# Kernel tuning notes

Measured on AMD Instinct MI355X. Metric: run time of the kernel, lower is better.

Reference implementation:

```python
import jax, jax.numpy as jnp
import numpy as np

B, S, DIM = 2, 512, 4096
SMAX = 4096
HQ, HKV, HD = 32, 8, 128
REP = HQ // HKV
THETA = 1e6
NEG = -1e9  # stands in for -inf in the causal mask (safe under softmax/vjp)


def setup_inputs() -> dict:
    key = jax.random.key(0)
    ks = jax.random.split(key, 8)
    x = jax.random.normal(ks[0], (B, S, DIM), jnp.float32)
    # RoPE tables (complex freqs_cis represented as cos/sin), rope_theta=1e6
    inv = 1.0 / (THETA ** (np.arange(0, HD, 2, dtype=np.float64) / HD))
    ang = np.arange(SMAX, dtype=np.float64)[:, None] * inv[None, :]
    freqs_cos = jnp.asarray(np.cos(ang), jnp.float32)  # [SMAX, HD//2]
    freqs_sin = jnp.asarray(np.sin(ang), jnp.float32)
    cache = jax.random.normal(ks[1], (2, 1, B, SMAX, HKV, HD), jnp.float32) * 0.02
    i = np.arange(SMAX)
    mask = jnp.asarray(np.where(i[None, :] <= i[:, None], 0.0, NEG), jnp.float32)
    storage_idx = jnp.arange(S, dtype=jnp.int32)
    sc = 0.02
    wq = jax.random.normal(ks[2], (HQ * HD, DIM), jnp.float32) * sc
    wk = jax.random.normal(ks[3], (HKV * HD, DIM), jnp.float32) * sc
    wv = jax.random.normal(ks[4], (HKV * HD, DIM), jnp.float32) * sc
    wo = jax.random.normal(ks[5], (DIM, HQ * HD), jnp.float32) * sc
    return {"x": x, "freqs_cos": freqs_cos, "freqs_sin": freqs_sin, "cache": cache,
            "mask": mask, "storage_idx": storage_idx, "wq": wq, "wk": wk, "wv": wv, "wo": wo}


def _rope(t, c, s):
    # t: [B,S,H,HD]; consecutive pairs (2i, 2i+1) form complex numbers
    tr = t.reshape(*t.shape[:-1], -1, 2)
    a, b = tr[..., 0], tr[..., 1]
    o0 = a * c - b * s
    o1 = a * s + b * c
    return jnp.stack([o0, o1], axis=-1).reshape(t.shape)


def reference(x, freqs_cos, freqs_sin, cache, mask, storage_idx, wq, wk, wv, wo):
    bsz, seqlen, _ = x.shape
    hd = cache.shape[-1]
    hkv = cache.shape[-2]
    hq = wq.shape[0] // hd
    rep = hq // hkv
    xq = (x @ wq.T).reshape(bsz, seqlen, hq, hd)
    xk = (x @ wk.T).reshape(bsz, seqlen, hkv, hd)
    xv = (x @ wv.T).reshape(bsz, seqlen, hkv, hd)
    c = freqs_cos[storage_idx][None, :, None, :]  # [1,S,1,HD//2]
    s = freqs_sin[storage_idx][None, :, None, :]
    xq = _rope(xq, c, s)
    xk = _rope(xk, c, s)
    # rotating-cache write (index_copy along seq dim of cache[0/1, li])
    k_cache = cache[0, 0].at[:, storage_idx].set(xk)  # [B,SMAX,HKV,HD]
    v_cache = cache[1, 0].at[:, storage_idx].set(xv)
    keys = jnp.repeat(k_cache, rep, axis=2)    # GQA expand -> [B,SMAX,HQ,HD]
    values = jnp.repeat(v_cache, rep, axis=2)
    # NOTE: faithful to source: scores = QK^T / (head_dim ** -0.5)
    scores = jnp.einsum('bqhd,bkhd->bhqk', xq, keys) / (hd ** -0.5)
    scores = scores + mask[storage_idx][None, None, :, :]
    probs = jax.nn.softmax(scores.astype(jnp.float32), axis=-1).astype(xq.dtype)
    out = jnp.einsum('bhqk,bkhd->bqhd', probs, values).reshape(bsz, seqlen, hq * hd)
    return out @ wo.T
```

## Files before the change

kernel.cpp:

```cpp
#include <hip/hip_runtime.h>

#define Bn   2
#define Sn   512
#define DIMn 4096
#define HQn  32
#define HKVn 8
#define HDn  128
#define NPAIR 64
#define KVN  (HKVn * HDn)
#define NALL (DIMn + 2 * KVN)
#define SCALE 11.313708498984761f

typedef short bf16x8 __attribute__((ext_vector_type(8)));
typedef float f32x4 __attribute__((ext_vector_type(4)));
typedef unsigned short ushort8 __attribute__((ext_vector_type(8)));
typedef int i32x4 __attribute__((ext_vector_type(4)));

__device__ __forceinline__ unsigned short f2bf_rne(float f) {
  unsigned u = __builtin_bit_cast(unsigned, f);
  u += 0x7fffu + ((u >> 16) & 1u);
  return (unsigned short)(u >> 16);
}
__device__ __forceinline__ float bf2f(unsigned short h) {
  unsigned u = ((unsigned)h) << 16;
  return __builtin_bit_cast(float, u);
}
__device__ __forceinline__ void split_bf16(float x, unsigned short& hi, unsigned short& lo) {
  unsigned u = __builtin_bit_cast(unsigned, x);
  hi = (unsigned short)(u >> 16);
  float hf = __builtin_bit_cast(float, u & 0xffff0000u);
  lo = (unsigned short)(__builtin_bit_cast(unsigned, x - hf) >> 16);
}
__device__ __forceinline__ void gload16(const void* g, void* lds) {
  __builtin_amdgcn_global_load_lds(
      (const __attribute__((address_space(1))) unsigned int*)g,
      (__attribute__((address_space(3))) unsigned int*)lds, 16, 0, 0);
}

__global__ __launch_bounds__(256) void quant_rows(
    const float* __restrict__ x, const float* __restrict__ wq,
    const float* __restrict__ wk, const float* __restrict__ wv,
    signed char* __restrict__ xh8, signed char* __restrict__ xl8,
    signed char* __restrict__ wh8, signed char* __restrict__ wl8,
    float* __restrict__ sA, float* __restrict__ sW)
{
  const int r = blockIdx.x;
  const int t = threadIdx.x;
  const float* src; signed char* ph; signed char* pl; float* ps; size_t prow;
  if (r < 1024) {
    src = x + (size_t)r * DIMn; ph = xh8; pl = xl8; ps = sA + r; prow = (size_t)r * DIMn;
  } else {
    int wr_ = r - 1024;
    ps = sW + wr_; ph = wh8; pl = wl8; prow = (size_t)wr_ * DIMn;
    if (wr_ < DIMn)            src = wq + (size_t)wr_ * DIMn;
    else if (wr_ < DIMn + KVN) src = wk + (size_t)(wr_ - DIMn) * DIMn;
    else                       src = wv + (size_t)(wr_ - DIMn - KVN) * DIMn;
  }
  float4 v[4];
  float am = 0.f;
  #pragma unroll
  for (int j = 0; j < 4; ++j) {
    v[j] = ((const float4*)src)[t + j * 256];
    am = fmaxf(am, fmaxf(fmaxf(fabsf(v[j].x), fabsf(v[j].y)),
                         fmaxf(fabsf(v[j].z), fabsf(v[j].w))));
  }
  #pragma unroll
  for (int o = 1; o < 64; o <<= 1) am = fmaxf(am, __shfl_xor(am, o));
  __shared__ float wm[4];
  if ((t & 63) == 0) wm[t >> 6] = am;
  __syncthreads();
  am = fmaxf(fmaxf(wm[0], wm[1]), fmaxf(wm[2], wm[3]));
  const float inv = (am > 0.f) ? 32512.0f / am : 0.f;
  if (t == 0) *ps = am * (1.0f / 32512.0f);
  #pragma unroll
  for (int j = 0; j < 4; ++j) {
    float fv[4] = {v[j].x, v[j].y, v[j].z, v[j].w};
    signed char hh[4], ll[4];
    #pragma unroll
    for (int e = 0; e < 4; ++e) {
      int q = __float2int_rn(fv[e] * inv);
      int hi = (q + 128) >> 8;
      hh[e] = (signed char)hi;
      ll[e] = (signed char)(q - (hi << 8));
    }
    ((char4*)(ph + prow))[t + j * 256] = make_char4(hh[0], hh[1], hh[2], hh[3]);
    ((char4*)(pl + prow))[t + j * 256] = make_char4(ll[0], ll[1], ll[2], ll[3]);
  }
}

__global__ void conv_plain_k(const float* __restrict__ s, unsigned short* __restrict__ hi, int n8)
{
  for (int i = blockIdx.x * blockDim.x + threadIdx.x; i < n8; i += gridDim.x * blockDim.x) {
    float4 a = ((const float4*)s)[2 * i];
    float4 b = ((const float4*)s)[2 * i + 1];
    float xv[8] = {a.x, a.y, a.z, a.w, b.x, b.y, b.z, b.w};
    ushort8 h;
    #pragma unroll
    for (int j = 0; j < 8; ++j) h[j] = f2bf_rne(xv[j]);
    ((ushort8*)hi)[i] = h;
  }
}

__global__ __launch_bounds__(256, 2) void qkv_gemm_i8(
    const signed char* __restrict__ Ah, const signed char* __restrict__ Al,
    const signed char* __restrict__ Wh, const signed char* __restrict__ Wl,
    const float* __restrict__ sA, const float* __restrict__ sW,
    float* __restrict__ CQ, float* __restrict__ CK, unsigned short* __restrict__ CV)
{
  constexpr int KS = 64;
  constexpr int TILEB = 224 * 128;
  __shared__ __align__(16) signed char Ls[2][TILEB];

  const int t = threadIdx.x, w = t >> 6, lane = t & 63;
  const int bid = blockIdx.x;
  const int s = (bid & 7) * 64 + (bid >> 3);
  const int bx = s >> 3, by = s & 7;
  const int bm = by * 128, bn = bx * 96;

  const signed char* gsrc[7];
  int ldst[7];
  #pragma unroll
  for (int j = 0; j < 4; ++j) {
    int u = j * 256 + t;
    int R = u >> 3, slot = u & 7;
    int q = slot ^ (R & 7);
    gsrc[j] = (q < 4 ? Ah : Al) + (size_t)(bm + R) * DIMn + (q & 3) * 16;
    ldst[j] = u * 16;
  }
  #pragma unroll
  for (int j = 4; j < 7; ++j) {
    int rb;
    if (j == 4)      rb = (t >> 3);
    else if (j == 5) rb = 48 + (t >> 3);
    else             rb = ((t < 128) ? 32 : 64) + (t >> 3);
    int slot = t & 7;
    int q = slot ^ (rb & 7);
    gsrc[j] = (q < 4 ? Wh : Wl) + (size_t)(bn + rb) * DIMn + (q & 3) * 16;
    ldst[j] = (128 + rb) * 128 + slot * 16;
  }

  const int wr = w >> 1, wc = w & 1;
  const int rl = lane & 15, kh = lane >> 4;
  int aoff[4], boff[3];
  #pragma unroll
  for (int fm = 0; fm < 4; ++fm) {
    int R = wr * 64 + fm * 16 + rl;
    aoff[fm] = R * 128 + ((kh ^ (R & 7)) * 16);
  }
  #pragma unroll
  for (int fn = 0; fn < 3; ++fn) {
    int R = 128 + wc * 48 + fn * 16 + rl;
    boff[fn] = R * 128 + ((kh ^ (R & 7)) * 16);
  }

  i32x4 acc1[4][3], acc2[4][3];
  #pragma unroll
  for (int i = 0; i < 4; ++i)
  #pragma unroll
    for (int j = 0; j < 3; ++j) {
      acc1[i][j] = (i32x4){0, 0, 0, 0};
      acc2[i][j] = (i32x4){0, 0, 0, 0};
    }

  const int nt = DIMn / KS;
  #pragma unroll
  for (int j = 0; j < 7; ++j) gload16(gsrc[j], &Ls[0][ldst[j]]);

  for (int tt = 0; tt < nt; ++tt) {
    const int buf = tt & 1, nbuf = buf ^ 1;
    const bool more = (tt + 1 < nt);

    asm volatile("s_waitcnt vmcnt(1)" ::: "memory");
    __builtin_amdgcn_s_barrier();
    __builtin_amdgcn_sched_barrier(0);
    if (more) {
      #pragma unroll
      for (int j = 0; j < 6; ++j)
        gload16(gsrc[j] + (size_t)(tt + 1) * KS, &Ls[nbuf][ldst[j]]);
    }
    const signed char* Lp = &Ls[buf][0];
    i32x4 ah[4], al[4];
    #pragma unroll
    for (int fm = 0; fm < 4; ++fm) {
      ah[fm] = *(const i32x4*)(Lp + aoff[fm]);
      al[fm] = *(const i32x4*)(Lp + (aoff[fm] ^ 64));
    }
    {
      i32x4 bh[2], bl[2];
      #pragma unroll
      for (int fn = 0; fn < 2; ++fn) {
        bh[fn] = *(const i32x4*)(Lp + boff[fn]);
        bl[fn] = *(const i32x4*)(Lp + (boff[fn] ^ 64));
      }
      __builtin_amdgcn_s_setprio(1);
      #pragma unroll
      for (int fm = 0; fm < 4; ++fm)
      #pragma unroll
        for (int fn = 0; fn < 2; ++fn) {
          acc1[fm][fn] = __builtin_amdgcn_mfma_i32_16x16x64_i8(ah[fm], bh[fn], acc1[fm][fn], 0, 0, 0);
          acc2[fm][fn] = __builtin_amdgcn_mfma_i32_16x16x64_i8(ah[fm], bl[fn], acc2[fm][fn], 0, 0, 0);
          acc2[fm][fn] = __builtin_amdgcn_mfma_i32_16x16x64_i8(al[fm], bh[fn], acc2[fm][fn], 0, 0, 0);
        }
      __builtin_amdgcn_s_setprio(0);
    }

    if (more) asm volatile("s_waitcnt vmcnt(6)" ::: "memory");
    else      asm volatile("s_waitcnt vmcnt(0)" ::: "memory");
    __builtin_amdgcn_s_barrier();
    __builtin_amdgcn_sched_barrier(0);
    if (more)
      gload16(gsrc[6] + (size_t)(tt + 1) * KS, &Ls[nbuf][ldst[6]]);
    {
      i32x4 bh = *(const i32x4*)(Lp + boff[2]);
      i32x4 bl = *(const i32x4*)(Lp + (boff[2] ^ 64));
      __builtin_amdgcn_s_setprio(1);
      #pragma unroll
      for (int fm = 0; fm < 4; ++fm) {
        acc1[fm][2] = __builtin_amdgcn_mfma_i32_16x16x64_i8(ah[fm], bh, acc1[fm][2], 0, 0, 0);
        acc2[fm][2] = __builtin_amdgcn_mfma_i32_16x16x64_i8(ah[fm], bl, acc2[fm][2], 0, 0, 0);
        acc2[fm][2] = __builtin_amdgcn_mfma_i32_16x16x64_i8(al[fm], bh, acc2[fm][2], 0, 0, 0);
      }
      __builtin_amdgcn_s_setprio(0);
    }
  }

  #pragma unroll
  for (int fn = 0; fn < 3; ++fn) {
    const int colW = bn + wc * 48 + fn * 16 + rl;
    const float sw = sW[colW];
    #pragma unroll
    for (int fm = 0; fm < 4; ++fm) {
      #pragma unroll
      for (int j = 0; j < 4; ++j) {
        int grow = bm + wr * 64 + fm * 16 + kh * 4 + j;
        float val = sA[grow] * sw *
            fmaf((float)acc1[fm][fn][j], 65536.0f, (float)acc2[fm][fn][j] * 256.0f);
        if (colW < DIMn)            CQ[(size_t)grow * DIMn + colW] = val;
        else if (colW < DIMn + KVN) CK[(size_t)grow * KVN + (colW - DIMn)] = val;
        else                        CV[(size_t)grow * KVN + (colW - DIMn - KVN)] = f2bf_rne(val);
      }
    }
  }
}

template<bool SPLIT, int OMODE>
__global__ __launch_bounds__(256, 2) void pgemm3(
    const unsigned short* __restrict__ Ah, const unsigned short* __restrict__ Al,
    const unsigned short* __restrict__ Wh, const unsigned short* __restrict__ Wl,
    void* __restrict__ C0, void* __restrict__ C1, void* __restrict__ C2, int Kd)
{
  constexpr int BM = 128, BN = 64;
  constexpr int ROWS = BM + BN;
  constexpr int UPT = ROWS / 32;
  constexpr int KS = SPLIT ? 32 : 64;
  constexpr int TILEB = ROWS * 128;

  __shared__ __align__(16) unsigned char Ls[3 * TILEB];

  const int t = threadIdx.x, w = t >> 6, lane = t & 63;
  const int bid = blockIdx.x;
  const int s = (bid & 7) * 64 + (bid >> 3);
  const int bm = (s & 7) * BM, bn = (s >> 3) * BN;

  const unsigned short* gsrc[UPT];
  #pragma unroll
  for (int j = 0; j < UPT; ++j) {
    int u = j * 256 + t;
    int R = u >> 3;
    int q = (u & 7) ^ (R & 7);
    int chunk = SPLIT ? (q & 3) : q;
    bool lo_ = SPLIT && (q >= 4);
    const unsigned short* base = (R < BM) ? (lo_ ? Al : Ah) : (lo_ ? Wl : Wh);
    int rg = (R < BM) ? (bm + R) : (bn + (R - BM));
    gsrc[j] = base + (size_t)rg * Kd + chunk * 8;
  }

  const int wr = w >> 1, wc = w & 1;
  const int rl = lane & 15, kh = lane >> 4;
  int aoff[4], boff[2];
  #pragma unroll
  for (int fm = 0; fm < 4; ++fm) {
    int r = wr * 64 + fm * 16 + rl;
    aoff[fm] = r * 128 + ((kh ^ (r & 7)) * 16);
  }
  #pragma unroll
  for (int fn = 0; fn < 2; ++fn) {
    int r = BM + wc * 32 + fn * 16 + rl;
    boff[fn] = r * 128 + ((kh ^ (r & 7)) * 16);
  }

  f32x4 acc[4][2];
  #pragma unroll
  for (int i = 0; i < 4; ++i)
  #pragma unroll
    for (int j = 0; j < 2; ++j) acc[i][j] = (f32x4){0.f, 0.f, 0.f, 0.f};

  const int nt = Kd / KS;
  #pragma unroll
  for (int j = 0; j < UPT; ++j) gload16(gsrc[j], &Ls[0 * TILEB + (j * 256 + t) * 16]);
  #pragma unroll
  for (int j = 0; j < UPT; ++j) gload16(gsrc[j] + KS, &Ls[1 * TILEB + (j * 256 + t) * 16]);

  int cur = 0;
  for (int tt = 0; tt < nt; ++tt) {
    if (tt + 1 < nt) asm volatile("s_waitcnt vmcnt(%0)" :: "n"(UPT) : "memory");
    else             asm volatile("s_waitcnt vmcnt(0)" ::: "memory");
    __builtin_amdgcn_s_barrier();
    __builtin_amdgcn_sched_barrier(0);

    int pre = cur + 2; if (pre >= 3) pre -= 3;
    if (tt + 2 < nt) {
      #pragma unroll
      for (int j = 0; j < UPT; ++j)
        gload16(gsrc[j] + (size_t)(tt + 2) * KS, &Ls[pre * TILEB + (j * 256 + t) * 16]);
    }

    const unsigned char* Lp = &Ls[cur * TILEB];
    bf16x8 a0[4], a1[4], b0[2], b1[2];
    #pragma unroll
    for (int fm = 0; fm < 4; ++fm) {
      a0[fm] = *(const bf16x8*)(Lp + aoff[fm]);
      a1[fm] = *(const bf16x8*)(Lp + (aoff[fm] ^ 64));
    }
    #pragma unroll
    for (int fn = 0; fn < 2; ++fn) {
      b0[fn] = *(const bf16x8*)(Lp + boff[fn]);
      b1[fn] = *(const bf16x8*)(Lp + (boff[fn] ^ 64));
    }
    __builtin_amdgcn_s_setprio(1);
    #pragma unroll
    for (int fm = 0; fm < 4; ++fm)
    #pragma unroll
      for (int fn = 0; fn < 2; ++fn) {
        if constexpr (SPLIT) {
          acc[fm][fn] = __builtin_amdgcn_mfma_f32_16x16x32_bf16(a0[fm], b0[fn], acc[fm][fn], 0, 0, 0);
          acc[fm][fn] = __builtin_amdgcn_mfma_f32_16x16x32_bf16(a1[fm], b0[fn], acc[fm][fn], 0, 0, 0);
          acc[fm][fn] = __builtin_amdgcn_mfma_f32_16x16x32_bf16(a0[fm], b1[fn], acc[fm][fn], 0, 0, 0);
        } else {
          acc[fm][fn] = __builtin_amdgcn_mfma_f32_16x16x32_bf16(a0[fm], b0[fn], acc[fm][fn], 0, 0, 0);
          acc[fm][fn] = __builtin_amdgcn_mfma_f32_16x16x32_bf16(a1[fm], b1[fn], acc[fm][fn], 0, 0, 0);
        }
      }
    __builtin_amdgcn_s_setprio(0);
    cur += 1; if (cur >= 3) cur -= 3;
  }

  const int crow0 = bm + wr * 64 + kh * 4;
  #pragma unroll
  for (int fm = 0; fm < 4; ++fm)
  #pragma unroll
    for (int fn = 0; fn < 2; ++fn)
    #pragma unroll
      for (int j = 0; j < 4; ++j) {
        int row = crow0 + fm * 16 + j;
        float v = acc[fm][fn][j];
        int col = bn + wc * 32 + fn * 16 + rl;
        if constexpr (OMODE == 0) {
          ((float*)C0)[(size_t)row * DIMn + col] = v;
        } else {
          if (col < DIMn)
            ((float*)C0)[(size_t)row * DIMn + col] = v;
          else if (col < DIMn + KVN)
            ((float*)C1)[(size_t)row * KVN + (col - DIMn)] = v;
          else
            ((unsigned short*)C2)[(size_t)row * KVN + (col - DIMn - KVN)] = f2bf_rne(v);
        }
      }
}

template<bool SPLIT, int BN>
__global__ __launch_bounds__(256, 2) void gemm_mfma(
    const float* __restrict__ A,
    const float* __restrict__ W0, float* __restrict__ C0,
    const float* __restrict__ W1, float* __restrict__ C1,
    int Kd, int N)
{
  constexpr int BM = 64;
  constexpr int KSTEP = SPLIT ? 32 : 64;
  constexpr int CPR = SPLIT ? 4 : 8;
  constexpr int AUNITS = BM * KSTEP / 8;
  constexpr int UNITS  = (BM + BN) * KSTEP / 8;
  constexpr int UPT = UNITS / 256;
  constexpr int FN = BN / 32;
  constexpr int ROWS = BM + BN;

  __shared__ __align__(16) unsigned short Ls[2][ROWS * 64];

  const float* __restrict__ W = (blockIdx.z == 0) ? W0 : W1;
  float* __restrict__ Cp = (blockIdx.z == 0) ? C0 : C1;

  const int t  = threadIdx.x;
  const int bm = blockIdx.y * BM;
  const int bn = blockIdx.x * BN;

  const float* gsrc[UPT];
  int loff[UPT];
  #pragma unroll
  for (int i = 0; i < UPT; ++i) {
    int u = i * 256 + t;
    int row, c;
    if (u < AUNITS) {
      row = u / CPR; c = u % CPR;
      gsrc[i] = A + (size_t)(bm + row) * Kd + c * 8;
    } else {
      int v = u - AUNITS;
      int rr = v / CPR; c = v % CPR;
      row = BM + rr;
      gsrc[i] = W + (size_t)(bn + rr) * Kd + c * 8;
    }
    loff[i] = row * 64 + (c ^ (row & 7)) * 8;
  }

  const int lane = t & 63;
  const int w  = t >> 6;
  const int wr = w >> 1, wc = w & 1;
  const int rl = lane & 15, kh = lane >> 4;

  int aoff[2], boff[FN];
  #pragma unroll
  for (int fm = 0; fm < 2; ++fm) {
    int row = wr * 32 + fm * 16 + rl;
    aoff[fm] = row * 64 + (kh ^ (row & 7)) * 8;
  }
  #pragma unroll
  for (int fn = 0; fn < FN; ++fn) {
    int row = BM + wc * (BN / 2) + fn * 16 + rl;
    boff[fn] = row * 64 + (kh ^ (row & 7)) * 8;
  }

  f32x4 acc[2][FN];
  #pragma unroll
  for (int i = 0; i < 2; ++i)
  #pragma unroll
    for (int j = 0; j < FN; ++j) acc[i][j] = (f32x4){0.f, 0.f, 0.f, 0.f};

  float4 f0[UPT], f1[UPT];
  #pragma unroll
  for (int i = 0; i < UPT; ++i) {
    f0[i] = *(const float4*)(gsrc[i]);
    f1[i] = *(const float4*)(gsrc[i] + 4);
  }

  const int nt = Kd / KSTEP;
  for (int tt = 0; tt < nt; ++tt) {
    unsigned short* Lp = &Ls[tt & 1][0];
    #pragma unroll
    for (int i = 0; i < UPT; ++i) {
      float xv[8] = {f0[i].x, f0[i].y, f0[i].z, f0[i].w,
                     f1[i].x, f1[i].y, f1[i].z, f1[i].w};
      ushort8 hi, lo;
      #pragma unroll
      for (int j = 0; j < 8; ++j) {
        if constexpr (SPLIT) {
          unsigned short h_, l_;
          split_bf16(xv[j], h_, l_);
          hi[j] = h_; lo[j] = l_;
        } else {
          hi[j] = f2bf_rne(xv[j]);
          lo[j] = 0;
        }
      }
      *(ushort8*)(Lp + loff[i]) = hi;
      if constexpr (SPLIT)
        *(ushort8*)(((uintptr_t)(Lp + loff[i])) ^ 64) = lo;
    }
    if (tt + 1 < nt) {
      #pragma unroll
      for (int i = 0; i < UPT; ++i) {
        f0[i] = *(const float4*)(gsrc[i] + (size_t)(tt + 1) * KSTEP);
        f1[i] = *(const float4*)(gsrc[i] + (size_t)(tt + 1) * KSTEP + 4);
      }
    }
    __syncthreads();

    bf16x8 a0[2], a1[2], b0[FN], b1[FN];
    #pragma unroll
    for (int fm = 0; fm < 2; ++fm) {
      const unsigned short* p = Lp + aoff[fm];
      a0[fm] = *(const bf16x8*)p;
      a1[fm] = *(const bf16x8*)(((uintptr_t)p) ^ 64);
    }
    #pragma unroll
    for (int fn = 0; fn < FN; ++fn) {
      const unsigned short* p = Lp + boff[fn];
      b0[fn] = *(const bf16x8*)p;
      b1[fn] = *(const bf16x8*)(((uintptr_t)p) ^ 64);
    }
    #pragma unroll
    for (int fm = 0; fm < 2; ++fm)
    #pragma unroll
      for (int fn = 0; fn < FN; ++fn) {
        if constexpr (SPLIT) {
          acc[fm][fn] = __builtin_amdgcn_mfma_f32_16x16x32_bf16(a0[fm], b0[fn], acc[fm][fn], 0, 0, 0);
          acc[fm][fn] = __builtin_amdgcn_mfma_f32_16x16x32_bf16(a1[fm], b0[fn], acc[fm][fn], 0, 0, 0);
          acc[fm][fn] = __builtin_amdgcn_mfma_f32_16x16x32_bf16(a0[fm], b1[fn], acc[fm][fn], 0, 0, 0);
        } else {
          acc[fm][fn] = __builtin_amdgcn_mfma_f32_16x16x32_bf16(a0[fm], b0[fn], acc[fm][fn], 0, 0, 0);
          acc[fm][fn] = __builtin_amdgcn_mfma_f32_16x16x32_bf16(a1[fm], b1[fn], acc[fm][fn], 0, 0, 0);
        }
      }
  }

  const int crow0 = bm + wr * 32 + kh * 4;
  const int ccol0 = bn + wc * (BN / 2) + rl;
  #pragma unroll
  for (int fm = 0; fm < 2; ++fm)
  #pragma unroll
    for (int fn = 0; fn < FN; ++fn)
    #pragma unroll
      for (int j = 0; j < 4; ++j)
        Cp[(size_t)(crow0 + fm * 16 + j) * N + ccol0 + fn * 16] = acc[fm][fn][j];
}

#define KT 32

template<bool BF16IO>
__global__ __launch_bounds__(256, 2) void flash_attn_mfma(
    const float* __restrict__ Qg, const float* __restrict__ Kg, const void* __restrict__ Vgv,
    const float* __restrict__ fc, const float* __restrict__ fs,
    const int* __restrict__ sidx, void* __restrict__ Ov)
{
  const int bid = blockIdx.x;
  const int qt = bid & 7;
  const int h  = (bid >> 3) & 31;
  const int b  = bid >> 8;
  const int q0 = qt * 64;
  const int hk = h >> 2;

  __shared__ __align__(16) unsigned short Ks[2][2][32][128];
  __shared__ __align__(16) unsigned short Vt[2][128][40];

  const int t = threadIdx.x;
  const int w = t >> 6;
  const int lane = t & 63;
  const int rl = lane & 15;
  const int kh = lane >> 4;

  const int qrow = q0 + w * 16 + rl;
  const int qp = sidx[qrow];

  int kr[2], kc_[2];
  #pragma unroll
  for (int i = 0; i < 2; ++i) { int u = i * 256 + t; kr[i] = u >> 4; kc_[i] = u & 15; }
  const int kkv = t >> 3, dcv = t & 7;

  const int nkt = (q0 + 64) / KT;
  const int qmaxw = q0 + w * 16 + 15;

  float kreg[2][8]; float4 kc4[2], ks4[2];
  float vregf[16];
  ushort8 vregu[2];

  #pragma unroll
  for (int i = 0; i < 2; ++i) {
    const float* kp_ = Kg + ((size_t)(b * Sn + kr[i]) * HKVn + hk) * HDn + kc_[i] * 8;
    *(float4*)&kreg[i][0] = *(const float4*)kp_;
    *(float4*)&kreg[i][4] = *(const float4*)(kp_ + 4);
    int posk = sidx[kr[i]];
    kc4[i] = *(const float4*)(fc + (size_t)posk * NPAIR + kc_[i] * 4);
    ks4[i] = *(const float4*)(fs + (size_t)posk * NPAIR + kc_[i] * 4);
  }
  if constexpr (BF16IO) {
    const unsigned short* vp_ = (const unsigned short*)Vgv +
        ((size_t)(b * Sn + kkv) * HKVn + hk) * HDn + dcv * 16;
    vregu[0] = *(const ushort8*)vp_;
    vregu[1] = *(const ushort8*)(vp_ + 8);
  } else {
    const float* vp_ = (const float*)Vgv + ((size_t)(b * Sn + kkv) * HKVn + hk) * HDn + dcv * 16;
    #pragma unroll
    for (int i = 0; i < 4; ++i) *(float4*)&vregf[i * 4] = *(const float4*)(vp_ + i * 4);
  }

  bf16x8 qh[4], ql[4];
  {
    const float* qptr = Qg + ((size_t)(b * Sn + qrow) * HQn + h) * HDn;
    #pragma unroll
    for (int ds = 0; ds < 4; ++ds) {
      int d0 = ds * 32 + kh * 8;
      float4 u0 = *(const float4*)(qptr + d0);
      float4 u1 = *(const float4*)(qptr + d0 + 4);
      float4 c4 = *(const float4*)(fc + (size_t)qp * NPAIR + d0 / 2);
      float4 s4 = *(const float4*)(fs + (size_t)qp * NPAIR + d0 / 2);
      float v[8];
      v[0] = u0.x * c4.x - u0.y * s4.x;  v[1] = u0.x * s4.x + u0.y * c4.x;
      v[2] = u0.z * c4.y - u0.w * s4.y;  v[3] = u0.z * s4.y + u0.w * c4.y;
      v[4] = u1.x * c4.z - u1.y * s4.z;  v[5] = u1.x * s4.z + u1.y * c4.z;
      v[6] = u1.z * c4.w - u1.w * s4.w;  v[7] = u1.z * s4.w + u1.w * c4.w;
      #pragma unroll
      for (int j = 0; j < 8; ++j) {
        unsigned short h_, l_;
        split_bf16(v[j], h_, l_);
        qh[ds][j] = (short)h_; ql[ds][j] = (short)l_;
      }
    }
  }

  float m_run = -3.0e38f, l_run = 0.f;
  f32x4 acc_o[8];
  #pragma unroll
  for (int i = 0; i < 8; ++i) acc_o[i] = (f32x4){0.f, 0.f, 0.f, 0.f};

  for (int tt = 0; tt < nkt; ++tt) {
    const int kbase = tt * KT;
    const int buf = tt & 1;

    #pragma unroll
    for (int i = 0; i < 2; ++i) {
      float rv[8];
      rv[0] = kreg[i][0] * kc4[i].x - kreg[i][1] * ks4[i].x;
      rv[1] = kreg[i][0] * ks4[i].x + kreg[i][1] * kc4[i].x;
      rv[2] = kreg[i][2] * kc4[i].y - kreg[i][3] * ks4[i].y;
      rv[3] = kreg[i][2] * ks4[i].y + kreg[i][3] * kc4[i].y;
      rv[4] = kreg[i][4] * kc4[i].z - kreg[i][5] * ks4[i].z;
      rv[5] = kreg[i][4] * ks4[i].z + kreg[i][5] * kc4[i].z;
      rv[6] = kreg[i][6] * kc4[i].w - kreg[i][7] * ks4[i].w;
      rv[7] = kreg[i][6] * ks4[i].w + kreg[i][7] * kc4[i].w;
      ushort8 hi, lo;
      #pragma unroll
      for (int j = 0; j < 8; ++j) {
        unsigned short h_, l_;
        split_bf16(rv[j], h_, l_);
        hi[j] = h_; lo[j] = l_;
      }
      int slot = kc_[i] ^ (kr[i] & 15);
      *(ushort8*)&Ks[buf][0][kr[i]][slot * 8] = hi;
      *(ushort8*)&Ks[buf][1][kr[i]][slot * 8] = lo;
    }
    if constexpr (BF16IO) {
      #pragma unroll
      for (int i = 0; i < 8; ++i) {
        Vt[buf][dcv * 16 + i][kkv] = vregu[0][i];
        Vt[buf][dcv * 16 + 8 + i][kkv] = vregu[1][i];
      }
    } else {
      #pragma unroll
      for (int i = 0; i < 16; ++i)
        Vt[buf][dcv * 16 + i][kkv] = f2bf_rne(vregf[i]);
    }

    if (tt + 1 < nkt) {
      const int kb = kbase + KT;
      #pragma unroll
      for (int i = 0; i < 2; ++i) {
        const float* kp_ = Kg + ((size_t)(b * Sn + kb + kr[i]) * HKVn + hk) * HDn + kc_[i] * 8;
        *(float4*)&kreg[i][0] = *(const float4*)kp_;
        *(float4*)&kreg[i][4] = *(const float4*)(kp_ + 4);
        int posk = sidx[kb + kr[i]];
        kc4[i] = *(const float4*)(fc + (size_t)posk * NPAIR + kc_[i] * 4);
        ks4[i] = *(const float4*)(fs + (size_t)posk * NPAIR + kc_[i] * 4);
      }
      if constexpr (BF16IO) {
        const unsigned short* vp_ = (const unsigned short*)Vgv +
            ((size_t)(b * Sn + kb + kkv) * HKVn + hk) * HDn + dcv * 16;
        vregu[0] = *(const ushort8*)vp_;
        vregu[1] = *(const ushort8*)(vp_ + 8);
      } else {
        const float* vp_ = (const float*)Vgv + ((size_t)(b * Sn + kb + kkv) * HKVn + hk) * HDn + dcv * 16;
        #pragma unroll
        for (int i = 0; i < 4; ++i) *(float4*)&vregf[i * 4] = *(const float4*)(vp_ + i * 4);
      }
    }
    __syncthreads();

    if (kbase > qmaxw) continue;

    float p[8];
    #pragma unroll
    for (int fm = 0; fm < 2; ++fm) {
      f32x4 accs = (f32x4){0.f, 0.f, 0.f, 0.f};
      #pragma unroll
      for (int ds = 0; ds < 4; ++ds) {
        int slot = (ds * 4 + kh) ^ rl;
        bf16x8 kH = *(const bf16x8*)&Ks[buf][0][fm * 16 + rl][slot * 8];
        bf16x8 kL = *(const bf16x8*)&Ks[buf][1][fm * 16 + rl][slot * 8];
        accs = __builtin_amdgcn_mfma_f32_16x16x32_bf16(kH, qh[ds], accs, 0, 0, 0);
        accs = __builtin_amdgcn_mfma_f32_16x16x32_bf16(kL, qh[ds], accs, 0, 0, 0);
        accs = __builtin_amdgcn_mfma_f32_16x16x32_bf16(kH, ql[ds], accs, 0, 0, 0);
      }
      #pragma unroll
      for (int r = 0; r < 4; ++r) {
        int kp = kbase + fm * 16 + kh * 4 + r;
        p[fm * 4 + r] = accs[r] * SCALE + ((kp <= qp) ? 0.f : -1.0e9f);
      }
    }

    float tmax = p[0];
    #pragma unroll
    for (int i = 1; i < 8; ++i) tmax = fmaxf(tmax, p[i]);
    tmax = fmaxf(tmax, __shfl_xor(tmax, 16));
    tmax = fmaxf(tmax, __shfl_xor(tmax, 32));
    float m_new = fmaxf(m_run, tmax);
    float crs = __expf(m_run - m_new);
    m_run = m_new;
    float tsum = 0.f;
    bf16x8 pa;
    #pragma unroll
    for (int i = 0; i < 8; ++i) {
      float ev = __expf(p[i] - m_new);
      tsum += ev;
      pa[i] = (short)f2bf_rne(ev);
    }
    tsum += __shfl_xor(tsum, 16);
    tsum += __shfl_xor(tsum, 32);
    l_run = l_run * crs + tsum;

    float cq[4];
    #pragma unroll
    for (int r = 0; r < 4; ++r) cq[r] = __shfl(crs, kh * 4 + r);

    #pragma unroll
    for (int db = 0; db < 8; ++db) {
      short4 v0 = *(const short4*)&Vt[buf][db * 16 + rl][kh * 4];
      short4 v1 = *(const short4*)&Vt[buf][db * 16 + rl][16 + kh * 4];
      bf16x8 vb = {v0.x, v0.y, v0.z, v0.w, v1.x, v1.y, v1.z, v1.w};
      f32x4 a = acc_o[db];
      a[0] *= cq[0]; a[1] *= cq[1]; a[2] *= cq[2]; a[3] *= cq[3];
      acc_o[db] = __builtin_amdgcn_mfma_f32_16x16x32_bf16(pa, vb, a, 0, 0, 0);
    }
  }

  float lq[4];
  #pragma unroll
  for (int r = 0; r < 4; ++r) lq[r] = 1.0f / __shfl(l_run, kh * 4 + r);
  #pragma unroll
  for (int db = 0; db < 8; ++db)
  #pragma unroll
    for (int r = 0; r < 4; ++r) {
      int q = q0 + w * 16 + kh * 4 + r;
      size_t idx = ((size_t)(b * Sn + q) * HQn + h) * HDn + db * 16 + rl;
      float val = acc_o[db][r] * lq[r];
      if constexpr (BF16IO) ((unsigned short*)Ov)[idx] = f2bf_rne(val);
      else                  ((float*)Ov)[idx] = val;
    }
}

extern "C" void kernel_launch(void* const* d_in, const int* in_sizes, int n_in,
                              void* d_out, int out_size, void* d_ws, size_t ws_size,
                              hipStream_t stream)
{
  const float* x    = (const float*)d_in[0];
  const float* fc   = (const float*)d_in[1];
  const float* fs   = (const float*)d_in[2];
  const int*   sidx = (const int*)d_in[5];
  const float* wq   = (const float*)d_in[6];
  const float* wk   = (const float*)d_in[7];
  const float* wv   = (const float*)d_in[8];
  const float* wo   = (const float*)d_in[9];
  float* out = (float*)d_out;

  const int M = Bn * Sn;
  const size_t EX  = (size_t)M * DIMn;
  const size_t EW  = (size_t)DIMn * DIMn;
  const size_t EK  = (size_t)M * KVN;
  const size_t EX8 = EX;
  const size_t EW8 = (size_t)NALL * DIMn;

  char* p = (char*)d_ws;
  signed char* xh8 = (signed char*)p;        p += EX8;
  signed char* xl8 = (signed char*)p;        p += EX8;
  signed char* wh8 = (signed char*)p;        p += EW8;
  signed char* wl8 = (signed char*)p;        p += EW8;
  float* sA = (float*)p;                     p += 1024 * 4;
  float* sW = (float*)p;                     p += (size_t)NALL * 4;
  float* Qw = (float*)p;                     p += 4 * EX;
  float* Kw = (float*)p;                     p += 4 * EK;
  unsigned short* Vw = (unsigned short*)p;   p += 2 * EK;
  unsigned short* woh = (unsigned short*)p;  p += 2 * EW;
  unsigned short* Aw = (unsigned short*)p;   p += 2 * EX;
  const size_t NEED = (size_t)(p - (char*)d_ws);

  if (ws_size >= NEED) {
    quant_rows<<<1024 + NALL, 256, 0, stream>>>(
        x, wq, wk, wv, xh8, xl8, wh8, wl8, sA, sW);
    qkv_gemm_i8<<<512, 256, 0, stream>>>(
        xh8, xl8, wh8, wl8, sA, sW, Qw, Kw, Vw);
    conv_plain_k<<<1024, 256, 0, stream>>>(wo, woh, (int)(EW / 8));
    flash_attn_mfma<true><<<Bn * HQn * (Sn / 64), 256, 0, stream>>>(
        Qw, Kw, Vw, fc, fs, sidx, Aw);
    pgemm3<false, 0><<<512, 256, 0, stream>>>(
        Aw, Aw, woh, woh, out, nullptr, nullptr, DIMn);
  } else {
    float* Qw2 = (float*)d_ws;
    float* Kw2 = Qw2 + (size_t)M * HQn * HDn;
    float* Vw2 = Kw2 + (size_t)M * HKVn * HDn;
    float* Aw2 = Vw2 + (size_t)M * HKVn * HDn;
    gemm_mfma<true, 128><<<dim3(DIMn / 128, M / 64, 1), 256, 0, stream>>>(
        x, wq, Qw2, wq, Qw2, DIMn, DIMn);
    gemm_mfma<true, 64><<<dim3((HKVn * HDn) / 64, M / 64, 2), 256, 0, stream>>>(
        x, wk, Kw2, wv, Vw2, DIMn, HKVn * HDn);
    flash_attn_mfma<false><<<Bn * HQn * (Sn / 64), 256, 0, stream>>>(
        Qw2, Kw2, Vw2, fc, fs, sidx, Aw2);
    gemm_mfma<false, 128><<<dim3(DIMn / 128, M / 64, 1), 256, 0, stream>>>(
        Aw2, wo, out, wo, out, DIMn, DIMn);
  }
}
```

Baseline: 219.2 us.

## Fold wo bf16 conversion into quant kernel and split QKV GEMM into three load phases

Removes the separate conv_plain_k launch by adding extra blocks to quant_rows that convert wo rows to bf16, saving one kernel launch and its tail. The int8 QKV GEMM's per-K-step schedule is reorganized from two barrier phases to three, with B-tile loads redistributed into 16-row groups so each of the three N fragments gets its own wait/barrier and prefetch slot. This is meant to interleave global-to-LDS prefetch with MFMA work more finely, at the cost of an extra barrier per iteration and fragile hand-tuned vmcnt values.

```diff
diff --git a/kernel.cpp b/kernel.cpp
--- a/kernel.cpp
+++ b/kernel.cpp
@@ -14,6 +14,7 @@
 typedef short bf16x8 __attribute__((ext_vector_type(8)));
 typedef float f32x4 __attribute__((ext_vector_type(4)));
 typedef unsigned short ushort8 __attribute__((ext_vector_type(8)));
+typedef unsigned short ushort4s __attribute__((ext_vector_type(4)));
 typedef int i32x4 __attribute__((ext_vector_type(4)));
 
 __device__ __forceinline__ unsigned short f2bf_rne(float f) {
@@ -40,12 +41,30 @@
 __global__ __launch_bounds__(256) void quant_rows(
     const float* __restrict__ x, const float* __restrict__ wq,
     const float* __restrict__ wk, const float* __restrict__ wv,
+    const float* __restrict__ wo,
     signed char* __restrict__ xh8, signed char* __restrict__ xl8,
     signed char* __restrict__ wh8, signed char* __restrict__ wl8,
+    unsigned short* __restrict__ woh,
     float* __restrict__ sA, float* __restrict__ sW)
 {
   const int r = blockIdx.x;
   const int t = threadIdx.x;
+
+  if (r >= 1024 + NALL) {
+    int wr2 = r - 1024 - NALL;
+    const float* src = wo + (size_t)wr2 * DIMn;
+    unsigned short* dst = woh + (size_t)wr2 * DIMn;
+    #pragma unroll
+    for (int j = 0; j < 4; ++j) {
+      float4 v = ((const float4*)src)[t + j * 256];
+      ushort4s h;
+      h[0] = f2bf_rne(v.x); h[1] = f2bf_rne(v.y);
+      h[2] = f2bf_rne(v.z); h[3] = f2bf_rne(v.w);
+      ((ushort4s*)dst)[t + j * 256] = h;
+    }
+    return;
+  }
+
   const float* src; signed char* ph; signed char* pl; float* ps; size_t prow;
   if (r < 1024) {
     src = x + (size_t)r * DIMn; ph = xh8; pl = xl8; ps = sA + r; prow = (size_t)r * DIMn;
@@ -88,19 +107,6 @@
   }
 }
 
-__global__ void conv_plain_k(const float* __restrict__ s, unsigned short* __restrict__ hi, int n8)
-{
-  for (int i = blockIdx.x * blockDim.x + threadIdx.x; i < n8; i += gridDim.x * blockDim.x) {
-    float4 a = ((const float4*)s)[2 * i];
-    float4 b = ((const float4*)s)[2 * i + 1];
-    float xv[8] = {a.x, a.y, a.z, a.w, b.x, b.y, b.z, b.w};
-    ushort8 h;
-    #pragma unroll
-    for (int j = 0; j < 8; ++j) h[j] = f2bf_rne(xv[j]);
-    ((ushort8*)hi)[i] = h;
-  }
-}
-
 __global__ __launch_bounds__(256, 2) void qkv_gemm_i8(
     const signed char* __restrict__ Ah, const signed char* __restrict__ Al,
     const signed char* __restrict__ Wh, const signed char* __restrict__ Wl,
@@ -129,10 +135,8 @@
   }
   #pragma unroll
   for (int j = 4; j < 7; ++j) {
-    int rb;
-    if (j == 4)      rb = (t >> 3);
-    else if (j == 5) rb = 48 + (t >> 3);
-    else             rb = ((t < 128) ? 32 : 64) + (t >> 3);
+    int base0 = (j - 4) * 16;
+    int rb = base0 + (t >> 3) + ((t < 128) ? 0 : 32);
     int slot = t & 7;
     int q = slot ^ (rb & 7);
     gsrc[j] = (q < 4 ? Wh : Wl) + (size_t)(bn + rb) * DIMn + (q & 3) * 16;
@@ -169,38 +173,51 @@
   for (int tt = 0; tt < nt; ++tt) {
     const int buf = tt & 1, nbuf = buf ^ 1;
     const bool more = (tt + 1 < nt);
-
-    asm volatile("s_waitcnt vmcnt(1)" ::: "memory");
+    const signed char* Lp = &Ls[buf][0];
+    i32x4 ah[4], al[4];
+
+    asm volatile("s_waitcnt vmcnt(2)" ::: "memory");
     __builtin_amdgcn_s_barrier();
     __builtin_amdgcn_sched_barrier(0);
     if (more) {
       #pragma unroll
-      for (int j = 0; j < 6; ++j)
+      for (int j = 0; j < 5; ++j)
         gload16(gsrc[j] + (size_t)(tt + 1) * KS, &Ls[nbuf][ldst[j]]);
     }
-    const signed char* Lp = &Ls[buf][0];
-    i32x4 ah[4], al[4];
     #pragma unroll
     for (int fm = 0; fm < 4; ++fm) {
       ah[fm] = *(const i32x4*)(Lp + aoff[fm]);
       al[fm] = *(const i32x4*)(Lp + (aoff[fm] ^ 64));
     }
     {
-      i32x4 bh[2], bl[2];
-      #pragma unroll
-      for (int fn = 0; fn < 2; ++fn) {
-        bh[fn] = *(const i32x4*)(Lp + boff[fn]);
-        bl[fn] = *(const i32x4*)(Lp + (boff[fn] ^ 64));
-      }
+      i32x4 bh = *(const i32x4*)(Lp + boff[0]);
+      i32x4 bl = *(const i32x4*)(Lp + (boff[0] ^ 64));
       __builtin_amdgcn_s_setprio(1);
       #pragma unroll
-      for (int fm = 0; fm < 4; ++fm)
-      #pragma unroll
-        for (int fn = 0; fn < 2; ++fn) {
-          acc1[fm][fn] = __builtin_amdgcn_mfma_i32_16x16x64_i8(ah[fm], bh[fn], acc1[fm][fn], 0, 0, 0);
-          acc2[fm][fn] = __builtin_amdgcn_mfma_i32_16x16x64_i8(ah[fm], bl[fn], acc2[fm][fn], 0, 0, 0);
-          acc2[fm][fn] = __builtin_amdgcn_mfma_i32_16x16x64_i8(al[fm], bh[fn], acc2[fm][fn], 0, 0, 0);
-        }
+      for (int fm = 0; fm < 4; ++fm) {
+        acc1[fm][0] = __builtin_amdgcn_mfma_i32_16x16x64_i8(ah[fm], bh, acc1[fm][0], 0, 0, 0);
+        acc2[fm][0] = __builtin_amdgcn_mfma_i32_16x16x64_i8(ah[fm], bl, acc2[fm][0], 0, 0, 0);
+        acc2[fm][0] = __builtin_amdgcn_mfma_i32_16x16x64_i8(al[fm], bh, acc2[fm][0], 0, 0, 0);
+      }
+      __builtin_amdgcn_s_setprio(0);
+    }
+
+    if (more) asm volatile("s_waitcnt vmcnt(6)" ::: "memory");
+    else      asm volatile("s_waitcnt vmcnt(1)" ::: "memory");
+    __builtin_amdgcn_s_barrier();
+    __builtin_amdgcn_sched_barrier(0);
+    if (more)
+      gload16(gsrc[5] + (size_t)(tt + 1) * KS, &Ls[nbuf][ldst[5]]);
+    {
+      i32x4 bh = *(const i32x4*)(Lp + boff[1]);
+      i32x4 bl = *(const i32x4*)(Lp + (boff[1] ^ 64));
+      __builtin_amdgcn_s_setprio(1);
+      #pragma unroll
+      for (int fm = 0; fm < 4; ++fm) {
+        acc1[fm][1] = __builtin_amdgcn_mfma_i32_16x16x64_i8(ah[fm], bh, acc1[fm][1], 0, 0, 0);
+        acc2[fm][1] = __builtin_amdgcn_mfma_i32_16x16x64_i8(ah[fm], bl, acc2[fm][1], 0, 0, 0);
+        acc2[fm][1] = __builtin_amdgcn_mfma_i32_16x16x64_i8(al[fm], bh, acc2[fm][1], 0, 0, 0);
+      }
       __builtin_amdgcn_s_setprio(0);
     }
 
@@ -770,11 +787,10 @@
   const size_t NEED = (size_t)(p - (char*)d_ws);
 
   if (ws_size >= NEED) {
-    quant_rows<<<1024 + NALL, 256, 0, stream>>>(
-        x, wq, wk, wv, xh8, xl8, wh8, wl8, sA, sW);
+    quant_rows<<<1024 + NALL + DIMn, 256, 0, stream>>>(
+        x, wq, wk, wv, wo, xh8, xl8, wh8, wl8, woh, sA, sW);
     qkv_gemm_i8<<<512, 256, 0, stream>>>(
         xh8, xl8, wh8, wl8, sA, sW, Qw, Kw, Vw);
-    conv_plain_k<<<1024, 256, 0, stream>>>(wo, woh, (int)(EW / 8));
     flash_attn_mfma<true><<<Bn * HQn * (Sn / 64), 256, 0, stream>>>(
         Qw, Kw, Vw, fc, fs, sidx, Aw);
     pgemm3<false, 0><<<512, 256, 0, stream>>>(
```

Measured after the change: 215.9 us. About the same (-1.5%).
